# Kernel tuning notes

Measured on AMD Instinct MI355X. Metric: run time of the kernel, lower is better.

## Reference

```python
import jax, jax.numpy as jnp
import numpy as np

N_USERS, N_ITEMS, N_TOPICS = 200000, 100000, 100
N_NODES = N_USERS + N_ITEMS + N_TOPICS
N_EDGES = 5000000
DIM = 64
LAYERS = 3
BATCH = 16384


def setup_inputs() -> dict:
    key = jax.random.key(0)
    ks = jax.random.split(key, 8)
    users = jax.random.randint(ks[0], (BATCH,), 0, N_USERS, dtype=jnp.int64 if jax.config.jax_enable_x64 else jnp.int32)
    items = jax.random.randint(ks[1], (BATCH,), 0, N_ITEMS, dtype=jnp.int64 if jax.config.jax_enable_x64 else jnp.int32)
    edge_rows = jax.random.randint(ks[2], (N_EDGES,), 0, N_NODES, dtype=jnp.int32)
    edge_cols = jax.random.randint(ks[3], (N_EDGES,), 0, N_NODES, dtype=jnp.int32)
    # values ~ 1/deg to mimic the symmetric-normalized A_hat of LightGCN
    edge_vals = jax.random.uniform(ks[4], (N_EDGES,), dtype=jnp.float32) / 16.0
    user_emb = 0.1 * jax.random.normal(ks[5], (N_USERS, DIM), dtype=jnp.float32)
    item_emb = 0.1 * jax.random.normal(ks[6], (N_ITEMS, DIM), dtype=jnp.float32)
    topic_emb = 0.1 * jax.random.normal(ks[7], (N_TOPICS, DIM), dtype=jnp.float32)
    return {"users": users, "items": items, "edge_rows": edge_rows,
            "edge_cols": edge_cols, "edge_vals": edge_vals,
            "user_emb": user_emb, "item_emb": item_emb, "topic_emb": topic_emb}


def reference(users, items, edge_rows, edge_cols, edge_vals, user_emb, item_emb, topic_emb):
    n_users = user_emb.shape[0]
    n_nodes = n_users + item_emb.shape[0] + topic_emb.shape[0]
    # E^0 = [users; items; topics]
    h = jnp.concatenate([user_emb, item_emb, topic_emb], axis=0)  # [N, dim]
    acc = h
    for _ in range(LAYERS):
        # sparse A_hat @ h : gather source rows, scale by edge weight, scatter-add to dst
        msgs = edge_vals[:, None] * h[edge_cols]                  # [E, dim]
        h = jax.ops.segment_sum(msgs, edge_rows, num_segments=n_nodes)
        acc = acc + h
    out = acc / (LAYERS + 1)                                      # stack-mean over layers
    u = out[users]                                                # [B, dim]
    it = out[n_users + items]                                     # items offset into node table
    return jnp.sum(u * it, axis=1)                                # [B]
```

## Files before the change

### kernel.cpp

```cpp
#include <hip/hip_runtime.h>
#include <hip/hip_fp16.h>

#define N_USERS  200000
#define N_ITEMS  100000
#define N_TOPICS 100
#define N_NODES  (N_USERS + N_ITEMS + N_TOPICS)
#define DIM      64
#define BSHIFT   10
#define BROWS    (1 << BSHIFT)
#define NBUCKETS ((N_NODES + BROWS - 1) >> BSHIFT)
#define NROWS_PAD (NBUCKETS * BROWS)
#define COLMASK  0x7FFFF
#define NB       512
#define NBSHIFT  9
#define M_TOT    (NBUCKETS * NB)
#define SB       256
#define CH       ((M_TOT + SB - 1) / SB)
#define BUCKET_CAP 24576



__global__ void prep_kernel(const int* __restrict__ rows,
                            int* __restrict__ partial, int n_edges,
                            const float* __restrict__ uemb,
                            const float* __restrict__ iemb,
                            const float* __restrict__ temb,
                            ushort* __restrict__ h0) {
    __shared__ int h[NBUCKETS];
    if (blockIdx.x < NB) {
        for (int i = threadIdx.x; i < NBUCKETS; i += blockDim.x) h[i] = 0;
        __syncthreads();
        int stride = NB * blockDim.x;
        for (int e = blockIdx.x * blockDim.x + threadIdx.x; e < n_edges; e += stride)
            atomicAdd(&h[((unsigned)rows[e]) >> BSHIFT], 1);
        __syncthreads();
        for (int i = threadIdx.x; i < NBUCKETS; i += blockDim.x)
            partial[blockIdx.x * NBUCKETS + i] = h[i];
    } else {
        int g = (blockIdx.x - NB) * blockDim.x + threadIdx.x;
        long base = (long)g * 4;
        if (base >= (long)N_NODES * DIM) return;
        const float* src;
        long off;
        if (base < (long)N_USERS * DIM)                 { src = uemb; off = base; }
        else if (base < (long)(N_USERS + N_ITEMS) * DIM){ src = iemb; off = base - (long)N_USERS * DIM; }
        else                                            { src = temb; off = base - (long)(N_USERS + N_ITEMS) * DIM; }
        float4 v = *(const float4*)(src + off);
        __half2 a = __floats2half2_rn(v.x, v.y);
        __half2 b = __floats2half2_rn(v.z, v.w);
        uint2 o;
        o.x = *(unsigned*)&a;
        o.y = *(unsigned*)&b;
        ((uint2*)h0)[g] = o;
    }
}

__device__ __forceinline__ int phys_idx(int L) {
    return (L & (NB - 1)) * NBUCKETS + (L >> NBSHIFT);
}

__global__ void scanB1_kernel(const int* __restrict__ partial,
                              int* __restrict__ psum) {
    __shared__ int s[256];
    int tid = threadIdx.x;
    int c0 = blockIdx.x * CH;
    int c1 = min(M_TOT, c0 + CH);
    int sum = 0;
    for (int L = c0 + tid; L < c1; L += 256) sum += partial[phys_idx(L)];
    s[tid] = sum;
    __syncthreads();
    for (int off = 128; off > 0; off >>= 1) {
        if (tid < off) s[tid] += s[tid + off];
        __syncthreads();
    }
    if (tid == 0) psum[blockIdx.x] = s[0];
}

__global__ void scanB3_kernel(const int* __restrict__ partial,
                              const int* __restrict__ psum,
                              int* __restrict__ offs) {
    __shared__ int s[SB];
    __shared__ int tile[256];
    __shared__ int carry;
    int tid = threadIdx.x;
    s[tid] = (tid < blockIdx.x) ? psum[tid] : 0;
    __syncthreads();
    for (int off = 128; off > 0; off >>= 1) {
        if (tid < off) s[tid] += s[tid + off];
        __syncthreads();
    }
    if (tid == 0) carry = s[0];
    __syncthreads();
    int c0 = blockIdx.x * CH;
    int c1 = min(M_TOT, c0 + CH);
    for (int base = c0; base < c1; base += 256) {
        int L = base + tid;
        int v = (L < c1) ? partial[phys_idx(L)] : 0;
        tile[tid] = v;
        __syncthreads();
        for (int off = 1; off < 256; off <<= 1) {
            int t = (tid >= off) ? tile[tid - off] : 0;
            __syncthreads();
            tile[tid] += t;
            __syncthreads();
        }
        if (L < c1) offs[L] = carry + tile[tid] - v;
        __syncthreads();
        if (tid == 255) carry += tile[255];
        __syncthreads();
    }
}

__global__ void scatter1_kernel(const int* __restrict__ rows,
                                const int* __restrict__ cols,
                                const float* __restrict__ vals,
                                const int* __restrict__ offs,
                                int2* __restrict__ bkt_buf, int n_edges) {
    __shared__ int lpos[NBUCKETS];
    for (int i = threadIdx.x; i < NBUCKETS; i += blockDim.x)
        lpos[i] = offs[i * NB + blockIdx.x];
    __syncthreads();
    int stride = gridDim.x * blockDim.x;
    for (int e = blockIdx.x * blockDim.x + threadIdx.x; e < n_edges; e += stride) {
        int r = rows[e];
        int b = ((unsigned)r) >> BSHIFT;
        int pos = atomicAdd(&lpos[b], 1);
        int2 p;
        p.x = cols[e] | ((r & (BROWS - 1)) << 19);
        p.y = __float_as_int(vals[e]);
        bkt_buf[pos] = p;
    }
}

__device__ __forceinline__ int pad8(int x) { return (x + 7) & ~7; }

__global__ void scatter2_kernel(const int2* __restrict__ bkt_buf,
                                const int* __restrict__ offs,
                                int2* __restrict__ row_span,
                                int2* __restrict__ csr_cv, int n_edges) {
    __shared__ int lcnt[BROWS];
    __shared__ int lptr[BROWS];
    __shared__ int lfill[BROWS];
    __shared__ int s[512];
    int b = blockIdx.x;
    int t = threadIdx.x;
    int e0 = offs[b * NB];
    int e1 = (b == NBUCKETS - 1) ? n_edges : offs[(b + 1) * NB];
    lcnt[t]  = 0;
    lfill[t] = 0;
    __syncthreads();
    for (int e = e0 + t; e < e1; e += 1024)
        atomicAdd(&lcnt[((unsigned)bkt_buf[e].x) >> 19], 1);
    __syncthreads();
    if (t < 512) s[t] = pad8(lcnt[2 * t]) + pad8(lcnt[2 * t + 1]);
    __syncthreads();
    for (int off = 1; off < 512; off <<= 1) {
        int v = 0;
        if (t < 512 && t >= off) v = s[t - off];
        __syncthreads();
        if (t < 512) s[t] += v;
        __syncthreads();
    }
    if (t < 512) {
        int base = b * BUCKET_CAP + (t ? s[t - 1] : 0);
        int rbase = b << BSHIFT;
        int pe = pad8(lcnt[2 * t]);
        int po = pad8(lcnt[2 * t + 1]);
        int p_even = base;
        int p_odd  = base + pe;
        lptr[2 * t]     = p_even;
        lptr[2 * t + 1] = p_odd;
        int2 sp0; sp0.x = p_even; sp0.y = p_even + pe;
        int2 sp1; sp1.x = p_odd;  sp1.y = p_odd + po;
        row_span[rbase + 2 * t]     = sp0;
        row_span[rbase + 2 * t + 1] = sp1;
    }
    __syncthreads();
    for (int e = e0 + t; e < e1; e += 1024) {
        int2 p = bkt_buf[e];
        int delta = ((unsigned)p.x) >> 19;
        int pos = lptr[delta] + atomicAdd(&lfill[delta], 1);
        int2 cv;
        cv.x = p.x & COLMASK;
        cv.y = p.y;
        csr_cv[pos] = cv;
    }
    __syncthreads();
    {
        int c  = lcnt[t];
        int cp = pad8(c);
        int p  = lptr[t];
        int2 z; z.x = 0; z.y = 0;
        for (int k = c; k < cp; ++k) csr_cv[p + k] = z;
    }
}

__device__ __forceinline__ float4 fma_mix4(const ushort* __restrict__ h,
                                           int row, int l16, float w,
                                           float4 acc) {
    uint2 r = ((const uint2*)(h + (size_t)row * DIM))[l16];
    __half2 h01 = *(__half2*)&r.x;
    __half2 h23 = *(__half2*)&r.y;
    acc.x = __builtin_fmaf(__half2float(__low2half(h01)),  w, acc.x);
    acc.y = __builtin_fmaf(__half2float(__high2half(h01)), w, acc.y);
    acc.z = __builtin_fmaf(__half2float(__low2half(h23)),  w, acc.z);
    acc.w = __builtin_fmaf(__half2float(__high2half(h23)), w, acc.w);
    return acc;
}

__device__ __forceinline__ float4 batch8(const int2* __restrict__ csr_cv,
                                         const ushort* __restrict__ h_src,
                                         int p, int l16, float4 acc) {
    const int4* q = (const int4*)(csr_cv + p);
    int4 a = q[0], b = q[1], c = q[2], d = q[3];
    acc = fma_mix4(h_src, a.x, l16, __int_as_float(a.y), acc);
    acc = fma_mix4(h_src, a.z, l16, __int_as_float(a.w), acc);
    acc = fma_mix4(h_src, b.x, l16, __int_as_float(b.y), acc);
    acc = fma_mix4(h_src, b.z, l16, __int_as_float(b.w), acc);
    acc = fma_mix4(h_src, c.x, l16, __int_as_float(c.y), acc);
    acc = fma_mix4(h_src, c.z, l16, __int_as_float(c.w), acc);
    acc = fma_mix4(h_src, d.x, l16, __int_as_float(d.y), acc);
    acc = fma_mix4(h_src, d.z, l16, __int_as_float(d.w), acc);
    return acc;
}

#define NWAVES ((N_NODES + 3) / 4)

__global__ void spmv_csr_kernel(const int2* __restrict__ row_span,
                                const int2* __restrict__ csr_cv,
                                const ushort* __restrict__ h_src,
                                ushort* __restrict__ h_dst,
                                const int* __restrict__ users,
                                const int* __restrict__ items,
                                float* __restrict__ u_acc,
                                float* __restrict__ it_acc,
                                int B, int first) {
    int wave = (int)(((long)blockIdx.x * blockDim.x + threadIdx.x) >> 6);
    int lane = threadIdx.x & 63;
    int g    = lane >> 4;
    int l16  = lane & 15;
    if (wave < NWAVES) {
        int r    = wave * 4 + g;
        int rc   = min(r, N_NODES - 1);
        int2 sp  = row_span[rc];
        int p0   = sp.x;
        int len  = (r < N_NODES) ? (sp.y - sp.x) : 0;
        int m = max(len, __shfl_xor(len, 16, 64));
        m = max(m, __shfl_xor(m, 32, 64));
        float4 acc = make_float4(0.f, 0.f, 0.f, 0.f);
        for (int off = 0; off < m; off += 8) {
            if (off < len)
                acc = batch8(csr_cv, h_src, p0 + off, l16, acc);
        }
        if (r < N_NODES) {
            __half2 a = __floats2half2_rn(acc.x, acc.y);
            __half2 b = __floats2half2_rn(acc.z, acc.w);
            uint2 o;
            o.x = *(unsigned*)&a;
            o.y = *(unsigned*)&b;
            ((uint2*)(h_dst + (size_t)r * DIM))[l16] = o;
        }
    } else {
        int s = (wave - NWAVES) * 4 + g;
        if (s >= 2 * B) return;
        int node = (s < B) ? users[s] : (N_USERS + items[s - B]);
        uint2 hr = ((const uint2*)(h_src + (size_t)node * DIM))[l16];
        float2 a01 = __half22float2(*(__half2*)&hr.x);
        float2 a23 = __half22float2(*(__half2*)&hr.y);
        float* dst = (s < B) ? (u_acc + (size_t)s * DIM)
                             : (it_acc + (size_t)(s - B) * DIM);
        float4* p = (float4*)dst + l16;
        if (first) {
            *p = make_float4(a01.x, a01.y, a23.x, a23.y);
        } else {
            float4 o = *p;
            o.x += a01.x; o.y += a01.y; o.z += a23.x; o.w += a23.y;
            *p = o;
        }
    }
}

__global__ void spmv_batch_kernel(const int2* __restrict__ row_span,
                                  const int2* __restrict__ csr_cv,
                                  const ushort* __restrict__ h_src,
                                  const int* __restrict__ users,
                                  const int* __restrict__ items,
                                  float* __restrict__ u_acc,
                                  float* __restrict__ it_acc, int B) {
    int wave = (int)(((long)blockIdx.x * blockDim.x + threadIdx.x) >> 6);
    int lane = threadIdx.x & 63;
    int g    = lane >> 4;
    int l16  = lane & 15;
    int s    = wave * 4 + g;
    bool ok  = s < 2 * B;
    int node = 0;
    if (ok) node = (s < B) ? users[s] : (N_USERS + items[s - B]);
    float4 acc = make_float4(0.f, 0.f, 0.f, 0.f);
    if (ok) {
        uint2 hr = ((const uint2*)(h_src + (size_t)node * DIM))[l16];
        float2 a01 = __half22float2(*(__half2*)&hr.x);
        float2 a23 = __half22float2(*(__half2*)&hr.y);
        acc = make_float4(a01.x, a01.y, a23.x, a23.y);
    }
    int2 sp  = row_span[node];
    int p0   = sp.x;
    int len  = ok ? (sp.y - sp.x) : 0;
    int m = max(len, __shfl_xor(len, 16, 64));
    m = max(m, __shfl_xor(m, 32, 64));
    for (int off = 0; off < m; off += 8) {
        if (off < len)
            acc = batch8(csr_cv, h_src, p0 + off, l16, acc);
    }
    if (ok) {
        float* dst = (s < B) ? (u_acc + (size_t)s * DIM)
                             : (it_acc + (size_t)(s - B) * DIM);
        float4* p = (float4*)dst + l16;
        float4 old = *p;
        old.x += acc.x; old.y += acc.y; old.z += acc.z; old.w += acc.w;
        *p = old;
    }
}

__global__ void dot_kernel(const float* __restrict__ u_acc,
                           const float* __restrict__ it_acc,
                           float* __restrict__ out, int B) {
    int gid  = blockIdx.x * blockDim.x + threadIdx.x;
    int b    = gid >> 6;
    int lane = gid & 63;
    if (b >= B) return;
    float p = u_acc[(size_t)b * DIM + lane] * it_acc[(size_t)b * DIM + lane];
    #pragma unroll
    for (int off = 32; off > 0; off >>= 1)
        p += __shfl_down(p, off, 64);
    if (lane == 0) out[b] = p * (1.0f / 16.0f);
}

extern "C" void kernel_launch(void* const* d_in, const int* in_sizes, int n_in,
                              void* d_out, int out_size, void* d_ws, size_t ws_size,
                              hipStream_t stream) {
    const int*   users = (const int*)d_in[0];
    const int*   items = (const int*)d_in[1];
    const int*   erows = (const int*)d_in[2];
    const int*   ecols = (const int*)d_in[3];
    const float* evals = (const float*)d_in[4];
    const float* uemb  = (const float*)d_in[5];
    const float* iemb  = (const float*)d_in[6];
    const float* temb  = (const float*)d_in[7];
    float* out = (float*)d_out;

    const int n_edges = in_sizes[2];
    const int B       = in_sizes[0];

    const size_t h2bytes = (((size_t)N_NODES * DIM * 2 + 255) / 256) * 256;
    const size_t abytes  = (size_t)B * DIM * sizeof(float);
    const size_t spbytes = (((size_t)NROWS_PAD * 8 + 255) / 256) * 256;
    const size_t csrbytes= (size_t)NBUCKETS * BUCKET_CAP * 8;
    const size_t bkbytes = (size_t)n_edges * 8;
    const size_t mbytes  = (((size_t)M_TOT * 4 + 255) / 256) * 256;

    char* ws = (char*)d_ws;
    size_t off = 0;
    ushort* hA       = (ushort*)(ws + off); off += h2bytes;
    ushort* hB       = (ushort*)(ws + off); off += h2bytes;
    float*  u_acc    = (float*) (ws + off); off += abytes;
    float*  it_acc   = (float*) (ws + off); off += abytes;
    int2*   row_span = (int2*)  (ws + off); off += spbytes;
    int2*   csr_cv   = (int2*)  (ws + off); off += csrbytes;
    int2*   bkt_buf  = (int2*)  (ws + off); off += bkbytes;
    int*    partial  = (int*)   (ws + off); off += mbytes;
    int*    offs     = (int*)   (ws + off); off += mbytes;
    int*    psum     = (int*)   (ws + off); off += 4096;

    dim3 blk(256);
    dim3 blk512(512);
    dim3 blk1k(1024);

    const long n4 = (long)N_NODES * DIM / 4;
    const int  nconcat = (int)((n4 + 511) / 512);
    prep_kernel<<<NB + nconcat, blk512, 0, stream>>>(erows, partial, n_edges,
                                                     uemb, iemb, temb, hA);
    scanB1_kernel<<<SB, blk, 0, stream>>>(partial, psum);
    scanB3_kernel<<<SB, blk, 0, stream>>>(partial, psum, offs);
    scatter1_kernel<<<NB, blk512, 0, stream>>>(erows, ecols, evals, offs, bkt_buf, n_edges);
    scatter2_kernel<<<NBUCKETS, blk1k, 0, stream>>>(bkt_buf, offs, row_span,
                                                    csr_cv, n_edges);

    const int gwaves  = (2 * B + 3) / 4;
    const int fblocks = (int)(((long)(NWAVES + gwaves) * 64 + 255) / 256);
    spmv_csr_kernel<<<fblocks, blk, 0, stream>>>(row_span, csr_cv, hA, hB,
                                                 users, items, u_acc, it_acc, B, 1);
    spmv_csr_kernel<<<fblocks, blk, 0, stream>>>(row_span, csr_cv, hB, hA,
                                                 users, items, u_acc, it_acc, B, 0);
    const int bblocks = (int)(((long)gwaves * 64 + 255) / 256);
    spmv_batch_kernel<<<bblocks, blk, 0, stream>>>(row_span, csr_cv, hA,
                                                   users, items, u_acc, it_acc, B);

    dot_kernel<<<(B * 64 + 255) / 256, blk, 0, stream>>>(u_acc, it_acc, out, B);
}
```

Before: 520.1 us.

## Vectorize edge loads, fuse batch init into prep and dot into batch SpMV

```diff
diff --git a/kernel.cpp b/kernel.cpp
--- a/kernel.cpp
+++ b/kernel.cpp
@@ -16,6 +16,7 @@
 #define M_TOT    (NBUCKETS * NB)
 #define SB       256
 #define CH       ((M_TOT + SB - 1) / SB)
+#define NCONCAT  (((N_NODES * DIM / 4) + 511) / 512)
 #define BUCKET_CAP 24576
 
 
@@ -25,18 +26,32 @@
                             const float* __restrict__ uemb,
                             const float* __restrict__ iemb,
                             const float* __restrict__ temb,
-                            ushort* __restrict__ h0) {
+                            ushort* __restrict__ h0,
+                            const int* __restrict__ users,
+                            const int* __restrict__ items,
+                            float* __restrict__ u_acc,
+                            float* __restrict__ it_acc, int B) {
     __shared__ int h[NBUCKETS];
     if (blockIdx.x < NB) {
         for (int i = threadIdx.x; i < NBUCKETS; i += blockDim.x) h[i] = 0;
         __syncthreads();
         int stride = NB * blockDim.x;
-        for (int e = blockIdx.x * blockDim.x + threadIdx.x; e < n_edges; e += stride)
+        int gid0 = blockIdx.x * blockDim.x + threadIdx.x;
+        int n4 = n_edges >> 2;
+        const int4* r4 = (const int4*)rows;
+        for (int e = gid0; e < n4; e += stride) {
+            int4 v = r4[e];
+            atomicAdd(&h[((unsigned)v.x) >> BSHIFT], 1);
+            atomicAdd(&h[((unsigned)v.y) >> BSHIFT], 1);
+            atomicAdd(&h[((unsigned)v.z) >> BSHIFT], 1);
+            atomicAdd(&h[((unsigned)v.w) >> BSHIFT], 1);
+        }
+        for (int e = (n4 << 2) + gid0; e < n_edges; e += stride)
             atomicAdd(&h[((unsigned)rows[e]) >> BSHIFT], 1);
         __syncthreads();
         for (int i = threadIdx.x; i < NBUCKETS; i += blockDim.x)
             partial[blockIdx.x * NBUCKETS + i] = h[i];
-    } else {
+    } else if (blockIdx.x < NB + NCONCAT) {
         int g = (blockIdx.x - NB) * blockDim.x + threadIdx.x;
         long base = (long)g * 4;
         if (base >= (long)N_NODES * DIM) return;
@@ -52,6 +67,17 @@
         o.x = *(unsigned*)&a;
         o.y = *(unsigned*)&b;
         ((uint2*)h0)[g] = o;
+    } else {
+        int g = (blockIdx.x - NB - NCONCAT) * blockDim.x + threadIdx.x;
+        int b    = g >> 4;
+        int lane = g & 15;
+        if (b >= B) return;
+        int u  = users[b];
+        int it = items[b];
+        float4 uv = ((const float4*)(uemb + (size_t)u  * DIM))[lane];
+        float4 iv = ((const float4*)(iemb + (size_t)it * DIM))[lane];
+        ((float4*)(u_acc  + (size_t)b * DIM))[lane] = uv;
+        ((float4*)(it_acc + (size_t)b * DIM))[lane] = iv;
     }
 }
 
@@ -120,13 +146,35 @@
     for (int i = threadIdx.x; i < NBUCKETS; i += blockDim.x)
         lpos[i] = offs[i * NB + blockIdx.x];
     __syncthreads();
-    int stride = gridDim.x * blockDim.x;
-    for (int e = blockIdx.x * blockDim.x + threadIdx.x; e < n_edges; e += stride) {
-        int r = rows[e];
-        int b = ((unsigned)r) >> BSHIFT;
+    int stride = NB * blockDim.x;
+    int gid0 = blockIdx.x * blockDim.x + threadIdx.x;
+    int n4 = n_edges >> 2;
+    const int4*   r4 = (const int4*)rows;
+    const int4*   c4 = (const int4*)cols;
+    const float4* v4 = (const float4*)vals;
+    for (int e = gid0; e < n4; e += stride) {
+        int4 r = r4[e];
+        int4 c = c4[e];
+        float4 v = v4[e];
+        #pragma unroll
+        for (int j = 0; j < 4; ++j) {
+            int rr = (j == 0) ? r.x : (j == 1) ? r.y : (j == 2) ? r.z : r.w;
+            int cc = (j == 0) ? c.x : (j == 1) ? c.y : (j == 2) ? c.z : c.w;
+            float vv = (j == 0) ? v.x : (j == 1) ? v.y : (j == 2) ? v.z : v.w;
+            int b = ((unsigned)rr) >> BSHIFT;
+            int pos = atomicAdd(&lpos[b], 1);
+            int2 p;
+            p.x = cc | ((rr & (BROWS - 1)) << 19);
+            p.y = __float_as_int(vv);
+            bkt_buf[pos] = p;
+        }
+    }
+    for (int e = (n4 << 2) + gid0; e < n_edges; e += stride) {
+        int rr = rows[e];
+        int b = ((unsigned)rr) >> BSHIFT;
         int pos = atomicAdd(&lpos[b], 1);
         int2 p;
-        p.x = cols[e] | ((r & (BROWS - 1)) << 19);
+        p.x = cols[e] | ((rr & (BROWS - 1)) << 19);
         p.y = __float_as_int(vals[e]);
         bkt_buf[pos] = p;
     }
@@ -261,6 +309,7 @@
             ((uint2*)(h_dst + (size_t)r * DIM))[l16] = o;
         }
     } else {
+        if (first < 0) return;
         int s = (wave - NWAVES) * 4 + g;
         if (s >= 2 * B) return;
         int node = (s < B) ? users[s] : (N_USERS + items[s - B]);
@@ -270,31 +319,28 @@
         float* dst = (s < B) ? (u_acc + (size_t)s * DIM)
                              : (it_acc + (size_t)(s - B) * DIM);
         float4* p = (float4*)dst + l16;
-        if (first) {
-            *p = make_float4(a01.x, a01.y, a23.x, a23.y);
-        } else {
-            float4 o = *p;
-            o.x += a01.x; o.y += a01.y; o.z += a23.x; o.w += a23.y;
-            *p = o;
-        }
-    }
-}
-
-__global__ void spmv_batch_kernel(const int2* __restrict__ row_span,
-                                  const int2* __restrict__ csr_cv,
-                                  const ushort* __restrict__ h_src,
-                                  const int* __restrict__ users,
-                                  const int* __restrict__ items,
-                                  float* __restrict__ u_acc,
-                                  float* __restrict__ it_acc, int B) {
+        float4 o = *p;
+        o.x += a01.x; o.y += a01.y; o.z += a23.x; o.w += a23.y;
+        *p = o;
+    }
+}
+
+__global__ void spmv_batch_dot_kernel(const int2* __restrict__ row_span,
+                                      const int2* __restrict__ csr_cv,
+                                      const ushort* __restrict__ h_src,
+                                      const int* __restrict__ users,
+                                      const int* __restrict__ items,
+                                      const float* __restrict__ u_acc,
+                                      const float* __restrict__ it_acc,
+                                      float* __restrict__ out, int B) {
     int wave = (int)(((long)blockIdx.x * blockDim.x + threadIdx.x) >> 6);
     int lane = threadIdx.x & 63;
     int g    = lane >> 4;
     int l16  = lane & 15;
-    int s    = wave * 4 + g;
-    bool ok  = s < 2 * B;
+    int b    = wave * 2 + (g >> 1);
+    bool ok  = b < B;
     int node = 0;
-    if (ok) node = (s < B) ? users[s] : (N_USERS + items[s - B]);
+    if (ok) node = ((g & 1) == 0) ? users[b] : (N_USERS + items[b]);
     float4 acc = make_float4(0.f, 0.f, 0.f, 0.f);
     if (ok) {
         uint2 hr = ((const uint2*)(h_src + (size_t)node * DIM))[l16];
@@ -302,7 +348,7 @@
         float2 a23 = __half22float2(*(__half2*)&hr.y);
         acc = make_float4(a01.x, a01.y, a23.x, a23.y);
     }
-    int2 sp  = row_span[node];
+    int2 sp  = row_span[ok ? node : 0];
     int p0   = sp.x;
     int len  = ok ? (sp.y - sp.x) : 0;
     int m = max(len, __shfl_xor(len, 16, 64));
@@ -312,27 +358,21 @@
             acc = batch8(csr_cv, h_src, p0 + off, l16, acc);
     }
     if (ok) {
-        float* dst = (s < B) ? (u_acc + (size_t)s * DIM)
-                             : (it_acc + (size_t)(s - B) * DIM);
-        float4* p = (float4*)dst + l16;
-        float4 old = *p;
-        old.x += acc.x; old.y += acc.y; old.z += acc.z; old.w += acc.w;
-        *p = old;
-    }
-}
-
-__global__ void dot_kernel(const float* __restrict__ u_acc,
-                           const float* __restrict__ it_acc,
-                           float* __restrict__ out, int B) {
-    int gid  = blockIdx.x * blockDim.x + threadIdx.x;
-    int b    = gid >> 6;
-    int lane = gid & 63;
-    if (b >= B) return;
-    float p = u_acc[(size_t)b * DIM + lane] * it_acc[(size_t)b * DIM + lane];
-    #pragma unroll
-    for (int off = 32; off > 0; off >>= 1)
-        p += __shfl_down(p, off, 64);
-    if (lane == 0) out[b] = p * (1.0f / 16.0f);
+        const float* st = ((g & 1) == 0) ? (u_acc  + (size_t)b * DIM)
+                                         : (it_acc + (size_t)b * DIM);
+        float4 sv = ((const float4*)st)[l16];
+        acc.x += sv.x; acc.y += sv.y; acc.z += sv.z; acc.w += sv.w;
+    }
+    float px = __shfl_xor(acc.x, 16, 64);
+    float py = __shfl_xor(acc.y, 16, 64);
+    float pz = __shfl_xor(acc.z, 16, 64);
+    float pw = __shfl_xor(acc.w, 16, 64);
+    float p = acc.x * px + acc.y * py + acc.z * pz + acc.w * pw;
+    p += __shfl_down(p, 8, 16);
+    p += __shfl_down(p, 4, 16);
+    p += __shfl_down(p, 2, 16);
+    p += __shfl_down(p, 1, 16);
+    if (ok && (g & 1) == 0 && l16 == 0) out[b] = p * (1.0f / 16.0f);
 }
 
 extern "C" void kernel_launch(void* const* d_in, const int* in_sizes, int n_in,
@@ -375,10 +415,10 @@
     dim3 blk512(512);
     dim3 blk1k(1024);
 
-    const long n4 = (long)N_NODES * DIM / 4;
-    const int  nconcat = (int)((n4 + 511) / 512);
-    prep_kernel<<<NB + nconcat, blk512, 0, stream>>>(erows, partial, n_edges,
-                                                     uemb, iemb, temb, hA);
+    const int ginit = (B * 16 + 511) / 512;
+    prep_kernel<<<NB + NCONCAT + ginit, blk512, 0, stream>>>(
+        erows, partial, n_edges, uemb, iemb, temb, hA,
+        users, items, u_acc, it_acc, B);
     scanB1_kernel<<<SB, blk, 0, stream>>>(partial, psum);
     scanB3_kernel<<<SB, blk, 0, stream>>>(partial, psum, offs);
     scatter1_kernel<<<NB, blk512, 0, stream>>>(erows, ecols, evals, offs, bkt_buf, n_edges);
@@ -386,14 +426,15 @@
                                                     csr_cv, n_edges);
 
     const int gwaves  = (2 * B + 3) / 4;
-    const int fblocks = (int)(((long)(NWAVES + gwaves) * 64 + 255) / 256);
-    spmv_csr_kernel<<<fblocks, blk, 0, stream>>>(row_span, csr_cv, hA, hB,
-                                                 users, items, u_acc, it_acc, B, 1);
-    spmv_csr_kernel<<<fblocks, blk, 0, stream>>>(row_span, csr_cv, hB, hA,
+    const int blocks1 = (int)(((long)NWAVES * 64 + 255) / 256);
+    const int blocks2 = (int)(((long)(NWAVES + gwaves) * 64 + 255) / 256);
+    spmv_csr_kernel<<<blocks1, blk, 0, stream>>>(row_span, csr_cv, hA, hB,
+                                                 users, items, u_acc, it_acc, B, -1);
+    spmv_csr_kernel<<<blocks2, blk, 0, stream>>>(row_span, csr_cv, hB, hA,
                                                  users, items, u_acc, it_acc, B, 0);
-    const int bblocks = (int)(((long)gwaves * 64 + 255) / 256);
-    spmv_batch_kernel<<<bblocks, blk, 0, stream>>>(row_span, csr_cv, hA,
-                                                   users, items, u_acc, it_acc, B);
-
-    dot_kernel<<<(B * 64 + 255) / 256, blk, 0, stream>>>(u_acc, it_acc, out, B);
-}
+    const int bwaves  = (B + 1) / 2;
+    const int bblocks = (int)(((long)bwaves * 64 + 255) / 256);
+    spmv_batch_dot_kernel<<<bblocks, blk, 0, stream>>>(row_span, csr_cv, hA,
+                                                       users, items, u_acc, it_acc,
+                                                       out, B);
+}
```

New measurement: 502.6 us (median of 2 runs). -3.4%, faster.
